# Performance work log

Hardware: AMD Instinct MI355X
Metric: run time of the kernel (lower is better)

## Reference

```python
import jax, jax.numpy as jnp
import numpy as np

E = 128          # number of bot groups (envs)
NB = 256         # bots per group
DQ = DK = DV = 256
D = DQ + DK + DV # 768
COM_RANGE = 15.0
KV_NOISE = 0.05
NEG = -1000000.0


def setup_inputs() -> dict:
    key = jax.random.key(0)
    k1, k2, k3, k4 = jax.random.split(key, 4)
    N = E * NB
    qkv = jax.random.normal(k1, (N, D), dtype=jnp.float32)
    # audibility mask: [N_total, n_per_group]; mask[bot_slice] -> [n, n] per group
    mask = jax.random.bernoulli(k2, 0.9, (N, NB))
    # 2D positions in a 30x30 arena so ~half of pairs fall within com_range
    bot_pos = jax.random.uniform(k3, (N, 2), dtype=jnp.float32, minval=0.0, maxval=30.0)
    # kv noise: zero on the q part [:K_DIM], gaussian(std=kv_noise) on k,v part
    noise = jnp.concatenate(
        [jnp.zeros((N, DQ), jnp.float32),
         KV_NOISE * jax.random.normal(k4, (N, DK + DV), dtype=jnp.float32)],
        axis=-1)
    s = jnp.float32(0.0)  # nn.Parameter init
    return {"qkv": qkv, "mask": mask, "bot_pos": bot_pos, "noise": noise, "s": s}


def reference(qkv, mask, bot_pos, noise, s):
    # noise injection on k,v channels (noise is zero on q channels)
    qkv = qkv + noise
    scale_s = jnp.abs(s) + 1.0

    # all bot groups are equal-sized -> batch the per-slice loop as [E, NB, ...]
    qkv_g = qkv.reshape(E, NB, D)
    q = qkv_g[..., :DQ] * scale_s
    k = qkv_g[..., DQ:DQ + DK]
    v = qkv_g[..., DQ + DK:]

    # pairwise-distance range mask per group
    pos = bot_pos.reshape(E, NB, 2)
    bdiff = pos[:, None, :, :] - pos[:, :, None, :]          # [E, NB, NB, 2]
    range_mask = jnp.linalg.norm(bdiff, axis=-1) < COM_RANGE  # [E, NB, NB]

    audible = mask.reshape(E, NB, NB) & range_mask            # [E, NB, NB]

    # SDPA with additive mask (torch adds -1e6 where masked)
    scores = jnp.einsum('eqd,ekd->eqk', q, k) / jnp.sqrt(jnp.float32(DK))
    scores = scores + jnp.where(audible, 0.0, NEG)
    attn = jax.nn.softmax(scores, axis=-1)
    x = jnp.einsum('eqk,ekd->eqd', attn, v)                   # [E, NB, DV]

    # zero out bots that hear nobody
    x = x * audible.any(axis=-1, keepdims=True)
    return x.reshape(E * NB, DV)
```

## Files before the change

kernel.cpp:

```cpp
#include <hip/hip_runtime.h>
#include <hip/hip_bf16.h>
#include <stdint.h>


#define EE   128
#define NBB  256
#define DDIM 768
#define NEGV (-1000000.0f)

typedef __attribute__((ext_vector_type(8))) short short8;
typedef __attribute__((ext_vector_type(4))) float f32x4;

__device__ __forceinline__ unsigned short f2bf(float f){
  union { float f; unsigned u; } v; v.f = f;
  return (unsigned short)((v.u + 0x7FFFu + ((v.u >> 16) & 1u)) >> 16);
}

__device__ __forceinline__ void gload16(const void* g, void* l){
  __builtin_amdgcn_global_load_lds((const __attribute__((address_space(1))) unsigned*)g,
                                   (__attribute__((address_space(3))) unsigned*)l, 16, 0, 0);
}

__global__ void k_prep(const float* __restrict__ qkv, const float* __restrict__ noise,
                       const float* __restrict__ sp,
                       unsigned short* __restrict__ Qb, unsigned short* __restrict__ Kb,
                       unsigned short* __restrict__ Vt){
  __shared__ unsigned short tile[64 * 66];
  if(blockIdx.x < 2048){
    const float scale = fabsf(sp[0]) + 1.0f;
    const int total = EE * NBB * 128;
    const int stride = 2048 * 256;
    for(int idx = blockIdx.x * 256 + threadIdx.x; idx < total; idx += stride){
      const int n   = idx >> 7;
      const int col = (idx & 127) << 2;
      f32x4 v = *(const f32x4*)(qkv + (size_t)n * DDIM + col);
      if(col < 256){
        ushort4 o = make_ushort4(f2bf(v[0]*scale), f2bf(v[1]*scale),
                                 f2bf(v[2]*scale), f2bf(v[3]*scale));
        *(ushort4*)(Qb + (size_t)n * 256 + col) = o;
      } else {
        f32x4 nz = *(const f32x4*)(noise + (size_t)n * DDIM + col);
        ushort4 o = make_ushort4(f2bf(v[0]+nz[0]), f2bf(v[1]+nz[1]),
                                 f2bf(v[2]+nz[2]), f2bf(v[3]+nz[3]));
        *(ushort4*)(Kb + (size_t)n * 256 + (col - 256)) = o;
      }
    }
  } else {
    const int b = blockIdx.x - 2048;
    const int e = b >> 4, t4 = b & 15;
    const int k0 = (t4 >> 2) << 6, d0 = (t4 & 3) << 6;
    const int u = threadIdx.x & 15, r = threadIdx.x >> 4;
    #pragma unroll
    for(int i = 0; i < 4; ++i){
      const int kl = r + (i << 4);
      const size_t off = ((size_t)(e*NBB + k0 + kl)) * DDIM + 512 + d0 + (u << 2);
      f32x4 v  = *(const f32x4*)(qkv   + off);
      f32x4 nz = *(const f32x4*)(noise + off);
      const int base = kl * 66 + (u << 2);
      tile[base+0] = f2bf(v[0]+nz[0]); tile[base+1] = f2bf(v[1]+nz[1]);
      tile[base+2] = f2bf(v[2]+nz[2]); tile[base+3] = f2bf(v[3]+nz[3]);
    }
    __syncthreads();
    #pragma unroll
    for(int i = 0; i < 4; ++i){
      const int dl = r + (i << 4);
      unsigned short o0 = tile[(u*4+0)*66 + dl];
      unsigned short o1 = tile[(u*4+1)*66 + dl];
      unsigned short o2 = tile[(u*4+2)*66 + dl];
      unsigned short o3 = tile[(u*4+3)*66 + dl];
      *(ushort4*)(Vt + ((size_t)(e*NBB + d0 + dl)) * NBB + k0 + (u << 2)) =
          make_ushort4(o0, o1, o2, o3);
    }
  }
}

__global__ void k_audible(const unsigned char* __restrict__ m8, const int* __restrict__ m32,
                          const float* __restrict__ pos, unsigned* __restrict__ aud){
  __shared__ float px[NBB], py[NBB];
  const int widx = blockIdx.x * 256 + threadIdx.x;
  const int e = widx >> 11;
  {
    const float2 p = *(const float2*)(pos + ((size_t)e * NBB + threadIdx.x) * 2);
    px[threadIdx.x] = p.x; py[threadIdx.x] = p.y;
  }
  const unsigned probe = ((const unsigned*)m32)[threadIdx.x & 63];
  const int isInt = !__any(probe > 1u);
  __syncthreads();
  const int row = (widx >> 3) & 255;
  const int wj  = widx & 7;
  const float qx = px[row], qy = py[row];
  const size_t mbase = ((size_t)(e * NBB + row)) * NBB + wj * 32;
  unsigned w = 0u;
  if(isInt){
    #pragma unroll
    for(int i = 0; i < 8; ++i){
      const int4 mv = *(const int4*)(m32 + mbase + i * 4);
      const int mvals[4] = {mv.x, mv.y, mv.z, mv.w};
      #pragma unroll
      for(int j = 0; j < 4; ++j){
        const int kk = i * 4 + j;
        const int k  = wj * 32 + kk;
        const float dx = px[k] - qx, dy = py[k] - qy;
        const float d2 = __fadd_rn(__fmul_rn(dx, dx), __fmul_rn(dy, dy));
        if((mvals[j] != 0) && (sqrtf(d2) < 15.0f)) w |= 1u << kk;
      }
    }
  } else {
    #pragma unroll
    for(int i = 0; i < 2; ++i){
      const int4 mv = *(const int4*)(m8 + mbase + i * 16);
      const int mvals[4] = {mv.x, mv.y, mv.z, mv.w};
      #pragma unroll
      for(int j = 0; j < 4; ++j)
        #pragma unroll
        for(int b = 0; b < 4; ++b){
          const int kk = i * 16 + j * 4 + b;
          const int k  = wj * 32 + kk;
          const float dx = px[k] - qx, dy = py[k] - qy;
          const float d2 = __fadd_rn(__fmul_rn(dx, dx), __fmul_rn(dy, dy));
          if((((unsigned)mvals[j] >> (8 * b)) & 0xFFu) && (sqrtf(d2) < 15.0f)) w |= 1u << kk;
        }
    }
  }
  aud[widx] = w;
}

__launch_bounds__(256, 2)
__global__ void k_attn(const unsigned short* __restrict__ Qb,
                       const unsigned short* __restrict__ Kb,
                       const unsigned short* __restrict__ Vt,
                       const unsigned* __restrict__ aud,
                       float* __restrict__ out){
  extern __shared__ unsigned char smem[];
  unsigned short* ldsKV = (unsigned short*)smem;
  unsigned short* ldsP  = (unsigned short*)(smem + 32768);
  unsigned*       audL  = (unsigned*)(smem + 65536);

  const int bid = blockIdx.x;
  const int e   = ((bid & 7) << 4) + (bid >> 5);
  const int qq  = (bid >> 3) & 3;
  const int tid  = threadIdx.x;
  const int wave = tid >> 6;
  const int lane = tid & 63;
  const int g    = lane >> 4;
  const int u    = lane & 15;
  const int q0   = qq * 64 + wave * 16;
  const size_t ebase = (size_t)e * NBB;

  {
    const unsigned* src = aud + (ebase + (size_t)qq * 64) * 8;
    audL[tid]       = src[tid];
    audL[tid + 256] = src[tid + 256];
  }

  short8 qf[8];
  #pragma unroll
  for(int dk = 0; dk < 8; ++dk)
    qf[dk] = *(const short8*)(Qb + (ebase + q0 + u) * 256 + dk*32 + g*8);

  const f32x4 zero4 = {0.f, 0.f, 0.f, 0.f};
  f32x4 acc[16];
  #pragma unroll
  for(int nt = 0; nt < 16; ++nt) acc[nt] = zero4;

  #pragma unroll
  for(int kq = 0; kq < 4; ++kq){
    __syncthreads();
    {
      const unsigned short* base = Kb + (ebase + (size_t)kq * 64) * 256;
      #pragma unroll
      for(int i = 0; i < 8; ++i){
        const int lrow = wave*16 + i*2 + (lane >> 5);
        const int col  = ((lane & 31) * 8) ^ ((lrow & 7) << 3);
        gload16(base + (size_t)lrow * 256 + col, ldsKV + (wave*16 + i*2) * 256);
      }
    }
    __syncthreads();
    #pragma unroll
    for(int nth = 0; nth < 4; ++nth){
      const unsigned short* kr = ldsKV + (nth*16 + u) * 256;
      const int sw = (u & 7) << 3;
      #pragma unroll
      for(int dk = 0; dk < 8; ++dk){
        short8 kb = *(const short8*)(kr + ((dk*32 + g*8) ^ sw));
        acc[kq*4 + nth] = __builtin_amdgcn_mfma_f32_16x16x32_bf16(qf[dk], kb, acc[kq*4 + nth], 0, 0, 0);
      }
    }
  }

  unsigned anybits = 0u;
  unsigned short* Pw = ldsP + wave * 4096;
  #pragma unroll
  for(int r = 0; r < 4; ++r){
    const int qw = g*4 + r;
    unsigned w[8];
    #pragma unroll
    for(int j = 0; j < 8; ++j) w[j] = audL[(wave*16 + qw)*8 + j];
    const unsigned anyw = w[0]|w[1]|w[2]|w[3]|w[4]|w[5]|w[6]|w[7];
    anybits |= (anyw ? 1u : 0u) << r;
    float m = -3.0e38f;
    #pragma unroll
    for(int nt = 0; nt < 16; ++nt){
      const unsigned bit = (w[nt >> 1] >> (((nt & 1) << 4) + u)) & 1u;
      float s = acc[nt][r] * 0.0625f + (bit ? 0.0f : NEGV);
      acc[nt][r] = s;
      m = fmaxf(m, s);
    }
    #pragma unroll
    for(int d = 1; d < 16; d <<= 1) m = fmaxf(m, __shfl_xor(m, d));
    float ssum = 0.0f;
    #pragma unroll
    for(int nt = 0; nt < 16; ++nt){
      const float p = __expf(acc[nt][r] - m);
      acc[nt][r] = p;
      ssum += p;
    }
    #pragma unroll
    for(int d = 1; d < 16; d <<= 1) ssum += __shfl_xor(ssum, d);
    const float inv = 1.0f / ssum;
    const int swp = (qw & 7) << 3;
    #pragma unroll
    for(int nt = 0; nt < 16; ++nt)
      Pw[qw*256 + ((nt*16 + u) ^ swp)] = f2bf(acc[nt][r] * inv);
  }

  short8 pa[8];
  {
    const unsigned short* pr = Pw + u*256;
    const int swp = (u & 7) << 3;
    #pragma unroll
    for(int kt = 0; kt < 8; ++kt)
      pa[kt] = *(const short8*)(pr + ((kt*32 + g*8) ^ swp));
  }

  #pragma unroll
  for(int dqt = 0; dqt < 4; ++dqt){
    __syncthreads();
    {
      const unsigned short* base = Vt + (ebase + (size_t)dqt * 64) * 256;
      #pragma unroll
      for(int i = 0; i < 8; ++i){
        const int lrow = wave*16 + i*2 + (lane >> 5);
        const int col  = ((lane & 31) * 8) ^ ((lrow & 7) << 3);
        gload16(base + (size_t)lrow * 256 + col, ldsKV + (wave*16 + i*2) * 256);
      }
    }
    __syncthreads();
    f32x4 xacc[4];
    #pragma unroll
    for(int dt = 0; dt < 4; ++dt) xacc[dt] = zero4;
    #pragma unroll
    for(int dt = 0; dt < 4; ++dt){
      const unsigned short* vr = ldsKV + (dt*16 + u) * 256;
      const int sw = (u & 7) << 3;
      #pragma unroll
      for(int kt = 0; kt < 8; ++kt){
        short8 bv = *(const short8*)(vr + ((kt*32 + g*8) ^ sw));
        xacc[dt] = __builtin_amdgcn_mfma_f32_16x16x32_bf16(pa[kt], bv, xacc[dt], 0, 0, 0);
      }
    }
    #pragma unroll
    for(int r = 0; r < 4; ++r){
      const float zf = ((anybits >> r) & 1u) ? 1.0f : 0.0f;
      float* orow = out + (ebase + q0 + g*4 + r) * 256 + dqt*64;
      #pragma unroll
      for(int dt = 0; dt < 4; ++dt)
        orow[dt*16 + u] = xacc[dt][r] * zf;
    }
  }
}

extern "C" void kernel_launch(void* const* d_in, const int* in_sizes, int n_in,
                              void* d_out, int out_size, void* d_ws, size_t ws_size,
                              hipStream_t stream){
  (void)in_sizes; (void)n_in; (void)out_size;
  const float* qkv   = (const float*)d_in[0];
  const void*  mask  = d_in[1];
  const float* pos   = (const float*)d_in[2];
  const float* noise = (const float*)d_in[3];
  const float* sp    = (const float*)d_in[4];

  unsigned char* ws = (unsigned char*)d_ws;
  unsigned short* Qb = (unsigned short*)(ws);
  unsigned short* Kb = (unsigned short*)(ws + 16777216);
  unsigned short* Vt = (unsigned short*)(ws + 33554432);
  unsigned*       ad = (unsigned*)(ws + 50331648);
  float* outp = (float*)d_out;
  (void)ws_size;

  k_prep   <<<4096, 256, 0, stream>>>(qkv, noise, sp, Qb, Kb, Vt);
  k_audible<<<1024, 256, 0, stream>>>((const unsigned char*)mask, (const int*)mask, pos, ad);

  hipFuncSetAttribute((const void*)k_attn, hipFuncAttributeMaxDynamicSharedMemorySize, 67584);
  k_attn<<<512, 256, 67584, stream>>>(Qb, Kb, Vt, ad, outp);
}
```

Measured before the change: 77.66 us.

## Fuse Q/K conversion and audibility mask into attention kernel

Drops the separate Q/K bf16 conversion and the audibility kernel. The attention kernel now reads fp32 Q and K+noise directly, converts them in registers, and builds the mask bitwords in LDS from the mask and positions. Only the V transpose stays as a prep kernel, which saves two launches and the bf16 workspace round trip for Q and K. The first V tile load is issued before the softmax so it overlaps that work. In exchange the attention kernel reads fp32 K from global memory (each group's K is read four times, once per q-block), uses more LDS, and carries more work per block.

```diff
diff --git a/kernel.cpp b/kernel.cpp
--- a/kernel.cpp
+++ b/kernel.cpp
@@ -15,126 +15,59 @@
   union { float f; unsigned u; } v; v.f = f;
   return (unsigned short)((v.u + 0x7FFFu + ((v.u >> 16) & 1u)) >> 16);
 }
+__device__ __forceinline__ unsigned short cvt1(float f){
+  __hip_bfloat16 h = __float2bfloat16(f);
+  unsigned short u; __builtin_memcpy(&u, &h, 2); return u;
+}
 
 __device__ __forceinline__ void gload16(const void* g, void* l){
   __builtin_amdgcn_global_load_lds((const __attribute__((address_space(1))) unsigned*)g,
                                    (__attribute__((address_space(3))) unsigned*)l, 16, 0, 0);
 }
 
-__global__ void k_prep(const float* __restrict__ qkv, const float* __restrict__ noise,
+__global__ void k_prep_vt(const float* __restrict__ qkv, const float* __restrict__ noise,
+                          unsigned short* __restrict__ Vt){
+  __shared__ unsigned short tile[64 * 66];
+  const int b = blockIdx.x;
+  const int e = b >> 4, t4 = b & 15;
+  const int k0 = (t4 >> 2) << 6, d0 = (t4 & 3) << 6;
+  const int u = threadIdx.x & 15, r = threadIdx.x >> 4;
+  #pragma unroll
+  for(int i = 0; i < 4; ++i){
+    const int kl = r + (i << 4);
+    const size_t off = ((size_t)(e*NBB + k0 + kl)) * DDIM + 512 + d0 + (u << 2);
+    f32x4 v  = *(const f32x4*)(qkv   + off);
+    f32x4 nz = *(const f32x4*)(noise + off);
+    const int base = kl * 66 + (u << 2);
+    tile[base+0] = f2bf(v[0]+nz[0]); tile[base+1] = f2bf(v[1]+nz[1]);
+    tile[base+2] = f2bf(v[2]+nz[2]); tile[base+3] = f2bf(v[3]+nz[3]);
+  }
+  __syncthreads();
+  #pragma unroll
+  for(int i = 0; i < 4; ++i){
+    const int dl = r + (i << 4);
+    unsigned short o0 = tile[(u*4+0)*66 + dl];
+    unsigned short o1 = tile[(u*4+1)*66 + dl];
+    unsigned short o2 = tile[(u*4+2)*66 + dl];
+    unsigned short o3 = tile[(u*4+3)*66 + dl];
+    *(ushort4*)(Vt + ((size_t)(e*NBB + d0 + dl)) * NBB + k0 + (u << 2)) =
+        make_ushort4(o0, o1, o2, o3);
+  }
+}
+
+__launch_bounds__(256, 2)
+__global__ void k_attn(const float* __restrict__ qkv, const float* __restrict__ noise,
                        const float* __restrict__ sp,
-                       unsigned short* __restrict__ Qb, unsigned short* __restrict__ Kb,
-                       unsigned short* __restrict__ Vt){
-  __shared__ unsigned short tile[64 * 66];
-  if(blockIdx.x < 2048){
-    const float scale = fabsf(sp[0]) + 1.0f;
-    const int total = EE * NBB * 128;
-    const int stride = 2048 * 256;
-    for(int idx = blockIdx.x * 256 + threadIdx.x; idx < total; idx += stride){
-      const int n   = idx >> 7;
-      const int col = (idx & 127) << 2;
-      f32x4 v = *(const f32x4*)(qkv + (size_t)n * DDIM + col);
-      if(col < 256){
-        ushort4 o = make_ushort4(f2bf(v[0]*scale), f2bf(v[1]*scale),
-                                 f2bf(v[2]*scale), f2bf(v[3]*scale));
-        *(ushort4*)(Qb + (size_t)n * 256 + col) = o;
-      } else {
-        f32x4 nz = *(const f32x4*)(noise + (size_t)n * DDIM + col);
-        ushort4 o = make_ushort4(f2bf(v[0]+nz[0]), f2bf(v[1]+nz[1]),
-                                 f2bf(v[2]+nz[2]), f2bf(v[3]+nz[3]));
-        *(ushort4*)(Kb + (size_t)n * 256 + (col - 256)) = o;
-      }
-    }
-  } else {
-    const int b = blockIdx.x - 2048;
-    const int e = b >> 4, t4 = b & 15;
-    const int k0 = (t4 >> 2) << 6, d0 = (t4 & 3) << 6;
-    const int u = threadIdx.x & 15, r = threadIdx.x >> 4;
-    #pragma unroll
-    for(int i = 0; i < 4; ++i){
-      const int kl = r + (i << 4);
-      const size_t off = ((size_t)(e*NBB + k0 + kl)) * DDIM + 512 + d0 + (u << 2);
-      f32x4 v  = *(const f32x4*)(qkv   + off);
-      f32x4 nz = *(const f32x4*)(noise + off);
-      const int base = kl * 66 + (u << 2);
-      tile[base+0] = f2bf(v[0]+nz[0]); tile[base+1] = f2bf(v[1]+nz[1]);
-      tile[base+2] = f2bf(v[2]+nz[2]); tile[base+3] = f2bf(v[3]+nz[3]);
-    }
-    __syncthreads();
-    #pragma unroll
-    for(int i = 0; i < 4; ++i){
-      const int dl = r + (i << 4);
-      unsigned short o0 = tile[(u*4+0)*66 + dl];
-      unsigned short o1 = tile[(u*4+1)*66 + dl];
-      unsigned short o2 = tile[(u*4+2)*66 + dl];
-      unsigned short o3 = tile[(u*4+3)*66 + dl];
-      *(ushort4*)(Vt + ((size_t)(e*NBB + d0 + dl)) * NBB + k0 + (u << 2)) =
-          make_ushort4(o0, o1, o2, o3);
-    }
-  }
-}
-
-__global__ void k_audible(const unsigned char* __restrict__ m8, const int* __restrict__ m32,
-                          const float* __restrict__ pos, unsigned* __restrict__ aud){
-  __shared__ float px[NBB], py[NBB];
-  const int widx = blockIdx.x * 256 + threadIdx.x;
-  const int e = widx >> 11;
-  {
-    const float2 p = *(const float2*)(pos + ((size_t)e * NBB + threadIdx.x) * 2);
-    px[threadIdx.x] = p.x; py[threadIdx.x] = p.y;
-  }
-  const unsigned probe = ((const unsigned*)m32)[threadIdx.x & 63];
-  const int isInt = !__any(probe > 1u);
-  __syncthreads();
-  const int row = (widx >> 3) & 255;
-  const int wj  = widx & 7;
-  const float qx = px[row], qy = py[row];
-  const size_t mbase = ((size_t)(e * NBB + row)) * NBB + wj * 32;
-  unsigned w = 0u;
-  if(isInt){
-    #pragma unroll
-    for(int i = 0; i < 8; ++i){
-      const int4 mv = *(const int4*)(m32 + mbase + i * 4);
-      const int mvals[4] = {mv.x, mv.y, mv.z, mv.w};
-      #pragma unroll
-      for(int j = 0; j < 4; ++j){
-        const int kk = i * 4 + j;
-        const int k  = wj * 32 + kk;
-        const float dx = px[k] - qx, dy = py[k] - qy;
-        const float d2 = __fadd_rn(__fmul_rn(dx, dx), __fmul_rn(dy, dy));
-        if((mvals[j] != 0) && (sqrtf(d2) < 15.0f)) w |= 1u << kk;
-      }
-    }
-  } else {
-    #pragma unroll
-    for(int i = 0; i < 2; ++i){
-      const int4 mv = *(const int4*)(m8 + mbase + i * 16);
-      const int mvals[4] = {mv.x, mv.y, mv.z, mv.w};
-      #pragma unroll
-      for(int j = 0; j < 4; ++j)
-        #pragma unroll
-        for(int b = 0; b < 4; ++b){
-          const int kk = i * 16 + j * 4 + b;
-          const int k  = wj * 32 + kk;
-          const float dx = px[k] - qx, dy = py[k] - qy;
-          const float d2 = __fadd_rn(__fmul_rn(dx, dx), __fmul_rn(dy, dy));
-          if((((unsigned)mvals[j] >> (8 * b)) & 0xFFu) && (sqrtf(d2) < 15.0f)) w |= 1u << kk;
-        }
-    }
-  }
-  aud[widx] = w;
-}
-
-__launch_bounds__(256, 2)
-__global__ void k_attn(const unsigned short* __restrict__ Qb,
-                       const unsigned short* __restrict__ Kb,
+                       const unsigned char* __restrict__ m8, const int* __restrict__ m32,
+                       const float* __restrict__ pos,
                        const unsigned short* __restrict__ Vt,
-                       const unsigned* __restrict__ aud,
                        float* __restrict__ out){
   extern __shared__ unsigned char smem[];
   unsigned short* ldsKV = (unsigned short*)smem;
   unsigned short* ldsP  = (unsigned short*)(smem + 32768);
   unsigned*       audL  = (unsigned*)(smem + 65536);
+  float*          posx  = (float*)(smem + 67584);
+  float*          posy  = (float*)(smem + 68608);
 
   const int bid = blockIdx.x;
   const int e   = ((bid & 7) << 4) + (bid >> 5);
@@ -148,15 +81,68 @@
   const size_t ebase = (size_t)e * NBB;
 
   {
-    const unsigned* src = aud + (ebase + (size_t)qq * 64) * 8;
-    audL[tid]       = src[tid];
-    audL[tid + 256] = src[tid + 256];
-  }
-
+    const float2 p = *(const float2*)(pos + (ebase + tid) * 2);
+    posx[tid] = p.x; posy[tid] = p.y;
+  }
+  const unsigned probe = ((const unsigned*)m32)[tid & 63];
+  const int isInt = !__any(probe > 1u);
+  __syncthreads();
+  #pragma unroll
+  for(int h = 0; h < 2; ++h){
+    const int w   = tid + h * 256;
+    const int row = w >> 3;
+    const int j   = w & 7;
+    const float qx = posx[qq*64 + row], qy = posy[qq*64 + row];
+    const size_t mbase = (ebase + qq*64 + row) * NBB + j * 32;
+    unsigned wd = 0u;
+    if(isInt){
+      #pragma unroll
+      for(int i = 0; i < 8; ++i){
+        const int4 mv = *(const int4*)(m32 + mbase + i * 4);
+        const int mvals[4] = {mv.x, mv.y, mv.z, mv.w};
+        #pragma unroll
+        for(int jj = 0; jj < 4; ++jj){
+          const int kk = i * 4 + jj;
+          const int k  = j * 32 + kk;
+          const float dx = posx[k] - qx, dy = posy[k] - qy;
+          const float d2 = __fadd_rn(__fmul_rn(dx, dx), __fmul_rn(dy, dy));
+          if((mvals[jj] != 0) && (sqrtf(d2) < 15.0f)) wd |= 1u << kk;
+        }
+      }
+    } else {
+      #pragma unroll
+      for(int i = 0; i < 2; ++i){
+        const int4 mv = *(const int4*)(m8 + mbase + i * 16);
+        const int mvals[4] = {mv.x, mv.y, mv.z, mv.w};
+        #pragma unroll
+        for(int jj = 0; jj < 4; ++jj)
+          #pragma unroll
+          for(int b = 0; b < 4; ++b){
+            const int kk = i * 16 + jj * 4 + b;
+            const int k  = j * 32 + kk;
+            const float dx = posx[k] - qx, dy = posy[k] - qy;
+            const float d2 = __fadd_rn(__fmul_rn(dx, dx), __fmul_rn(dy, dy));
+            if((((unsigned)mvals[jj] >> (8 * b)) & 0xFFu) && (sqrtf(d2) < 15.0f)) wd |= 1u << kk;
+          }
+      }
+    }
+    audL[w] = wd;
+  }
+
+  const float scale = fabsf(sp[0]) + 1.0f;
   short8 qf[8];
-  #pragma unroll
-  for(int dk = 0; dk < 8; ++dk)
-    qf[dk] = *(const short8*)(Qb + (ebase + q0 + u) * 256 + dk*32 + g*8);
+  {
+    const float* qrow = qkv + (ebase + q0 + u) * DDIM;
+    #pragma unroll
+    for(int dk = 0; dk < 8; ++dk){
+      f32x4 a = *(const f32x4*)(qrow + dk*32 + g*8);
+      f32x4 b = *(const f32x4*)(qrow + dk*32 + g*8 + 4);
+      short8 f;
+      f[0]=cvt1(a[0]*scale); f[1]=cvt1(a[1]*scale); f[2]=cvt1(a[2]*scale); f[3]=cvt1(a[3]*scale);
+      f[4]=cvt1(b[0]*scale); f[5]=cvt1(b[1]*scale); f[6]=cvt1(b[2]*scale); f[7]=cvt1(b[3]*scale);
+      qf[dk] = f;
+    }
+  }
 
   const f32x4 zero4 = {0.f, 0.f, 0.f, 0.f};
   f32x4 acc[16];
@@ -167,12 +153,17 @@
   for(int kq = 0; kq < 4; ++kq){
     __syncthreads();
     {
-      const unsigned short* base = Kb + (ebase + (size_t)kq * 64) * 256;
-      #pragma unroll
-      for(int i = 0; i < 8; ++i){
-        const int lrow = wave*16 + i*2 + (lane >> 5);
-        const int col  = ((lane & 31) * 8) ^ ((lrow & 7) << 3);
-        gload16(base + (size_t)lrow * 256 + col, ldsKV + (wave*16 + i*2) * 256);
+      #pragma unroll
+      for(int i = 0; i < 16; ++i){
+        const int row = wave*16 + i;
+        const size_t goff = (ebase + kq*64 + row) * DDIM + 256 + lane*4;
+        f32x4 a  = *(const f32x4*)(qkv + goff);
+        f32x4 nz = *(const f32x4*)(noise + goff);
+        uint2 o;
+        o.x = (unsigned)cvt1(a[0]+nz[0]) | ((unsigned)cvt1(a[1]+nz[1]) << 16);
+        o.y = (unsigned)cvt1(a[2]+nz[2]) | ((unsigned)cvt1(a[3]+nz[3]) << 16);
+        const int col = (lane*4) ^ ((row & 7) << 3);
+        *(uint2*)(ldsKV + row*256 + col) = o;
       }
     }
     __syncthreads();
@@ -185,6 +176,17 @@
         short8 kb = *(const short8*)(kr + ((dk*32 + g*8) ^ sw));
         acc[kq*4 + nth] = __builtin_amdgcn_mfma_f32_16x16x32_bf16(qf[dk], kb, acc[kq*4 + nth], 0, 0, 0);
       }
+    }
+  }
+
+  __syncthreads();
+  {
+    const unsigned short* base = Vt + (ebase + 0) * 256;
+    #pragma unroll
+    for(int i = 0; i < 8; ++i){
+      const int lrow = wave*16 + i*2 + (lane >> 5);
+      const int col  = ((lane & 31) * 8) ^ ((lrow & 7) << 3);
+      gload16(base + (size_t)lrow * 256 + col, ldsKV + (wave*16 + i*2) * 256);
     }
   }
 
@@ -233,39 +235,40 @@
       pa[kt] = *(const short8*)(pr + ((kt*32 + g*8) ^ swp));
   }
 
+  __syncthreads();
   #pragma unroll
   for(int dqt = 0; dqt < 4; ++dqt){
-    __syncthreads();
-    {
-      const unsigned short* base = Vt + (ebase + (size_t)dqt * 64) * 256;
+    f32x4 xacc[4];
+    #pragma unroll
+    for(int dt = 0; dt < 4; ++dt) xacc[dt] = zero4;
+    #pragma unroll
+    for(int dt = 0; dt < 4; ++dt){
+      const unsigned short* vr = ldsKV + (dt*16 + u) * 256;
+      const int sw = (u & 7) << 3;
+      #pragma unroll
+      for(int kt = 0; kt < 8; ++kt){
+        short8 bv = *(const short8*)(vr + ((kt*32 + g*8) ^ sw));
+        xacc[dt] = __builtin_amdgcn_mfma_f32_16x16x32_bf16(pa[kt], bv, xacc[dt], 0, 0, 0);
+      }
+    }
+    #pragma unroll
+    for(int r = 0; r < 4; ++r){
+      const float zf = ((anybits >> r) & 1u) ? 1.0f : 0.0f;
+      float* orow = out + (ebase + q0 + g*4 + r) * 256 + dqt*64;
+      #pragma unroll
+      for(int dt = 0; dt < 4; ++dt)
+        orow[dt*16 + u] = xacc[dt][r] * zf;
+    }
+    if(dqt < 3){
+      __syncthreads();
+      const unsigned short* base = Vt + (ebase + (size_t)(dqt+1) * 64) * 256;
       #pragma unroll
       for(int i = 0; i < 8; ++i){
         const int lrow = wave*16 + i*2 + (lane >> 5);
         const int col  = ((lane & 31) * 8) ^ ((lrow & 7) << 3);
         gload16(base + (size_t)lrow * 256 + col, ldsKV + (wave*16 + i*2) * 256);
       }
-    }
-    __syncthreads();
-    f32x4 xacc[4];
-    #pragma unroll
-    for(int dt = 0; dt < 4; ++dt) xacc[dt] = zero4;
-    #pragma unroll
-    for(int dt = 0; dt < 4; ++dt){
-      const unsigned short* vr = ldsKV + (dt*16 + u) * 256;
-      const int sw = (u & 7) << 3;
-      #pragma unroll
-      for(int kt = 0; kt < 8; ++kt){
-        short8 bv = *(const short8*)(vr + ((kt*32 + g*8) ^ sw));
-        xacc[dt] = __builtin_amdgcn_mfma_f32_16x16x32_bf16(pa[kt], bv, xacc[dt], 0, 0, 0);
-      }
-    }
-    #pragma unroll
-    for(int r = 0; r < 4; ++r){
-      const float zf = ((anybits >> r) & 1u) ? 1.0f : 0.0f;
-      float* orow = out + (ebase + q0 + g*4 + r) * 256 + dqt*64;
-      #pragma unroll
-      for(int dt = 0; dt < 4; ++dt)
-        orow[dt*16 + u] = xacc[dt][r] * zf;
+      __syncthreads();
     }
   }
 }
@@ -273,24 +276,20 @@
 extern "C" void kernel_launch(void* const* d_in, const int* in_sizes, int n_in,
                               void* d_out, int out_size, void* d_ws, size_t ws_size,
                               hipStream_t stream){
-  (void)in_sizes; (void)n_in; (void)out_size;
+  (void)in_sizes; (void)n_in; (void)out_size; (void)ws_size;
   const float* qkv   = (const float*)d_in[0];
   const void*  mask  = d_in[1];
   const float* pos   = (const float*)d_in[2];
   const float* noise = (const float*)d_in[3];
   const float* sp    = (const float*)d_in[4];
 
-  unsigned char* ws = (unsigned char*)d_ws;
-  unsigned short* Qb = (unsigned short*)(ws);
-  unsigned short* Kb = (unsigned short*)(ws + 16777216);
-  unsigned short* Vt = (unsigned short*)(ws + 33554432);
-  unsigned*       ad = (unsigned*)(ws + 50331648);
+  unsigned short* Vt = (unsigned short*)d_ws;
   float* outp = (float*)d_out;
-  (void)ws_size;
-
-  k_prep   <<<4096, 256, 0, stream>>>(qkv, noise, sp, Qb, Kb, Vt);
-  k_audible<<<1024, 256, 0, stream>>>((const unsigned char*)mask, (const int*)mask, pos, ad);
-
-  hipFuncSetAttribute((const void*)k_attn, hipFuncAttributeMaxDynamicSharedMemorySize, 67584);
-  k_attn<<<512, 256, 67584, stream>>>(Qb, Kb, Vt, ad, outp);
-}
+
+  k_prep_vt<<<2048, 256, 0, stream>>>(qkv, noise, Vt);
+
+  hipFuncSetAttribute((const void*)k_attn, hipFuncAttributeMaxDynamicSharedMemorySize, 69632);
+  k_attn<<<512, 256, 69632, stream>>>(qkv, noise, sp,
+                                      (const unsigned char*)mask, (const int*)mask,
+                                      pos, Vt, outp);
+}
```

Result: faster. 66.90 us (-13.9%).
